# Optimization experiments

Measured on AMD Instinct MI355X. Metric: run time of the kernel, lower is better.

## Reference

```python
import jax, jax.numpy as jnp
import numpy as np

N_NODES = 100000
N_EDGES = 1600000
D_IN = 64
D_HID = 64


def setup_inputs() -> dict:
    key = jax.random.key(0)
    k1, k2, k3, k4, k5 = jax.random.split(key, 5)
    x = jax.random.normal(k1, (N_NODES, D_IN), dtype=jnp.float32)
    edge_index = jax.random.randint(k2, (2, N_EDGES), 0, N_NODES, dtype=jnp.int64)
    edge_weight = jax.random.uniform(k3, (N_EDGES,), dtype=jnp.float32)
    # GCNConv glorot-initialized linear weights (bias=False)
    s0 = (6.0 / (D_IN + D_HID)) ** 0.5
    W0 = jax.random.uniform(k4, (D_IN, D_HID), minval=-s0, maxval=s0, dtype=jnp.float32)
    s1 = (6.0 / (D_HID + D_HID)) ** 0.5
    W1 = jax.random.uniform(k5, (D_HID, D_HID), minval=-s1, maxval=s1, dtype=jnp.float32)
    return {"x": x, "edge_index": edge_index, "edge_weight": edge_weight, "W0": W0, "W1": W1}


def _gcn_layer(x, W, src, dst, edge_weight, deg_inv_sqrt, n_nodes):
    # h = X W  (bias=False)
    h = x @ W  # [N, D]
    # symmetric normalization including self-loops (weight 1)
    norm = deg_inv_sqrt[src] * edge_weight * deg_inv_sqrt[dst]  # [E]
    # gather src features, scale, scatter-sum at dst
    agg = jax.ops.segment_sum(norm[:, None] * h[src], dst, num_segments=n_nodes)
    # self-loop contribution: norm_ii = deg_inv_sqrt[i]^2 * 1
    agg = agg + (deg_inv_sqrt * deg_inv_sqrt)[:, None] * h
    return jax.nn.relu(agg)  # dropout is identity in eval mode


def reference(x, edge_index, edge_weight, W0, W1):
    src, dst = edge_index[0], edge_index[1]
    # degree with self-loops (self-loop weight = 1), aggregated at dst (source_to_target flow)
    deg = jax.ops.segment_sum(edge_weight, dst, num_segments=N_NODES) + 1.0
    deg_inv_sqrt = jax.lax.rsqrt(deg)
    x = _gcn_layer(x, W0, src, dst, edge_weight, deg_inv_sqrt, N_NODES)
    x = _gcn_layer(x, W1, src, dst, edge_weight, deg_inv_sqrt, N_NODES)
    return x
```

## Files before the change

kernel.cpp:

```cpp
#include <hip/hip_runtime.h>
#include <hip/hip_fp16.h>

#define D 64
#define BSH 9
#define BSZ (1 << BSH)
#define PB 4096
#define CAPR 10240
#define CAPU (2 * CAPR)
#define FASTU (BSZ * 32)
#define SCAP 9216

__global__ __launch_bounds__(256) void initcur(int* __restrict__ ccur, int nbuck) {
    int t = threadIdx.x;
    if (t < nbuck) ccur[t] = t * CAPR;
    if (t == 255) ccur[255] = 0;
}

__global__ __launch_bounds__(512) void bucket1(const int* __restrict__ src,
                                               const int* __restrict__ dst,
                                               const float* __restrict__ ew,
                                               int* __restrict__ ccur,
                                               int2* __restrict__ pairs2,
                                               int E, int nbuck) {
    __shared__ int hist[512];
    __shared__ int lbase[512];
    __shared__ int gbase[512];
    __shared__ int wsum[8];
    __shared__ int w0s[PB];
    __shared__ int w1s[PB];
    __shared__ unsigned char bids[PB];
    int t = threadIdx.x;
    hist[t] = 0;
    __syncthreads();
    int e0 = blockIdx.x * PB;
    int cnt = min(PB, E - e0);
    int b[8], lr[8], w0[8], w1[8];
    int i8 = t * 8;
    bool full8 = (i8 + 8 <= cnt);
    if (full8) {
        int4   sa = *(const int4*)&src[e0 + i8];
        int4   sb = *(const int4*)&src[e0 + i8 + 4];
        int4   da = *(const int4*)&dst[e0 + i8];
        int4   db = *(const int4*)&dst[e0 + i8 + 4];
        float4 wa = *(const float4*)&ew[e0 + i8];
        float4 wb = *(const float4*)&ew[e0 + i8 + 4];
        int ss[8] = {sa.x, sa.y, sa.z, sa.w, sb.x, sb.y, sb.z, sb.w};
        int ds[8] = {da.x, da.y, da.z, da.w, db.x, db.y, db.z, db.w};
        float wv[8] = {wa.x, wa.y, wa.z, wa.w, wb.x, wb.y, wb.z, wb.w};
#pragma unroll
        for (int k = 0; k < 8; ++k) {
            b[k]  = ds[k] >> BSH;
            w0[k] = ss[k] | ((ds[k] & (BSZ - 1)) << 17);
            w1[k] = __float_as_int(wv[k]);
            lr[k] = atomicAdd(&hist[b[k]], 1);
        }
    } else {
#pragma unroll
        for (int k = 0; k < 8; ++k) {
            int idx = i8 + k;
            if (idx < cnt) {
                int d = dst[e0 + idx];
                b[k]  = d >> BSH;
                w0[k] = src[e0 + idx] | ((d & (BSZ - 1)) << 17);
                w1[k] = __float_as_int(ew[e0 + idx]);
                lr[k] = atomicAdd(&hist[b[k]], 1);
            }
        }
    }
    __syncthreads();
    int hv = hist[t];
    int lane = t & 63, wv8 = t >> 6;
    int s = hv;
#pragma unroll
    for (int off = 1; off < 64; off <<= 1) {
        int u = __shfl_up(s, off, 64);
        if (lane >= off) s += u;
    }
    if (lane == 63) wsum[wv8] = s;
    __syncthreads();
    int woff = 0;
#pragma unroll
    for (int w = 0; w < 8; ++w) { int x = wsum[w]; if (w < wv8) woff += x; }
    int excl = s + woff - hv;
    lbase[t] = excl;
    if (t < nbuck && hv > 0) gbase[t] = atomicAdd(&ccur[t], hv);
    __syncthreads();
#pragma unroll
    for (int k = 0; k < 8; ++k) {
        int idx = i8 + k;
        if (idx < cnt) {
            int slot = lbase[b[k]] + lr[k];
            w0s[slot] = w0[k];
            w1s[slot] = w1[k];
            bids[slot] = (unsigned char)b[k];
        }
    }
    __syncthreads();
    for (int i = t; i < cnt; i += 512) {
        int bb = bids[i];
        int pos = gbase[bb] + (i - lbase[bb]);
        pairs2[pos] = make_int2(w0s[i], w1s[i]);
    }
}

__global__ __launch_bounds__(512) void sort2(int2* __restrict__ pairs2,
                                             unsigned int* __restrict__ fastU,
                                             const int* __restrict__ ccur,
                                             int2* __restrict__ extRng,
                                             unsigned int* __restrict__ extU,
                                             int* __restrict__ gext,
                                             float* __restrict__ dis,
                                             int N, int nbuck) {
    __shared__ int2 se[SCAP];
    __shared__ int cnt[512];
    __shared__ float sdeg[512];
    __shared__ int ebase[512];
    int b = blockIdx.x;
    int t = threadIdx.x;
    int baseR = b * CAPR;
    int baseU = b * CAPU;
    int cntb = min(ccur[b] - baseR, SCAP);
    for (int i = t; i < cntb; i += 512) se[i] = pairs2[baseR + i];
    cnt[t] = 0;
    sdeg[t] = 0.0f;
    __syncthreads();
    for (int i = t; i < cntb; i += 512) {
        int2 p = se[i];
        int dl = (p.x >> 17) & (BSZ - 1);
        int lr = atomicAdd(&cnt[dl], 1);
        atomicAdd(&sdeg[dl], __int_as_float(p.y));
        se[i].x = p.x | (lr << 26);
    }
    __syncthreads();
    int node = (b << BSH) + t;
    int cntv = cnt[t];
    int tot  = cntv + 1;
    int pc   = (tot <= 16) ? 16 : ((tot + 31) & ~31);
    int extLen = (pc > 32) ? (pc - 32) : 0;
    int extBase = 0;
    if (node < N && extLen > 0) extBase = atomicAdd(gext, extLen);
    float dloc = rsqrtf(sdeg[t] + 1.0f);
    __syncthreads();
    sdeg[t]  = dloc;
    ebase[t] = extBase;
    if (node < N) {
        int flag = (pc == 16) ? (1 << 30) : 0;
        extRng[node] = make_int2(extBase | flag, extBase + extLen);
        dis[node]    = dloc;
    }
    for (int i = t; i < FASTU; i += 512) fastU[baseU + i] = 0u;
    __syncthreads();
    for (int i = t; i < cntb; i += 512) {
        int2 p = se[i];
        int dl = (p.x >> 17) & (BSZ - 1);
        int s  = p.x & 0x1FFFF;
        int rank = ((unsigned int)p.x) >> 26;
        float w = __int_as_float(p.y) * sdeg[dl];
        unsigned int h = (unsigned int)__half_as_ushort(__float2half_rn(w));
        unsigned int packed = ((unsigned int)s << 15) | ((h + 1u) >> 1);
        if (rank < 32) fastU[baseU + dl * 32 + rank] = packed;
        else           extU[ebase[dl] + rank - 32]   = packed;
    }
    if (node < N) {
        unsigned int h = (unsigned int)__half_as_ushort(__float2half_rn(dloc));
        unsigned int selfp = ((unsigned int)node << 15) | ((h + 1u) >> 1);
        if (cntv < 32) fastU[baseU + t * 32 + cntv] = selfp;
        else           extU[extBase + cntv - 32]    = selfp;
        for (int i = cntv + 1 - 32; i < extLen; ++i) extU[extBase + i] = 0u;
    }
}

template<int HIN>
__global__ __launch_bounds__(256) void gemm64h(const void* __restrict__ Xv,
                                               const float* __restrict__ W,
                                               const float* __restrict__ dis,
                                               __half* __restrict__ Hb, int n) {
    __shared__ float Ws[64 * 64];
    __shared__ float Xs[16 * 64];
    for (int t = threadIdx.x; t < 64 * 64; t += 256) Ws[t] = W[t];
    int row0 = blockIdx.x * 16;
    for (int t = threadIdx.x; t < 16 * 64; t += 256) {
        int r = row0 + (t >> 6);
        float v = 0.0f;
        if (r < n) {
            if constexpr (HIN) v = __half2float(((const __half*)Xv)[r * 64 + (t & 63)]);
            else               v = ((const float*)Xv)[r * 64 + (t & 63)];
        }
        Xs[t] = v;
    }
    __syncthreads();
    int r  = threadIdx.x >> 4;
    int jc = (threadIdx.x & 15) * 4;
    float4 acc = make_float4(0.f, 0.f, 0.f, 0.f);
#pragma unroll
    for (int k = 0; k < 64; ++k) {
        float xv = Xs[r * 64 + k];
        float4 w = *(const float4*)&Ws[k * 64 + jc];
        acc.x += xv * w.x; acc.y += xv * w.y; acc.z += xv * w.z; acc.w += xv * w.w;
    }
    int rr = row0 + r;
    if (rr < n) {
        float ds = dis[rr];
        ushort4 pk;
        pk.x = __half_as_ushort(__float2half(ds * acc.x));
        pk.y = __half_as_ushort(__float2half(ds * acc.y));
        pk.z = __half_as_ushort(__float2half(ds * acc.z));
        pk.w = __half_as_ushort(__float2half(ds * acc.w));
        *(ushort4*)&Hb[rr * 64 + jc] = pk;
    }
}

__device__ __forceinline__ void acc_group(unsigned int pv, int g, int fl,
                                          const __half* __restrict__ Hb,
                                          __half2 a0[4], __half2 a1[4],
                                          __half2 a2[4], __half2 a3[4]) {
    unsigned int q0 = __shfl(pv, g, 64);
    unsigned int q1 = __shfl(pv, g + 8, 64);
    unsigned int q2 = __shfl(pv, g + 16, 64);
    unsigned int q3 = __shfl(pv, g + 24, 64);
    uint4 r0 = *(const uint4*)(Hb + (size_t)(q0 >> 15) * 64 + fl);
    uint4 r1 = *(const uint4*)(Hb + (size_t)(q1 >> 15) * 64 + fl);
    uint4 r2 = *(const uint4*)(Hb + (size_t)(q2 >> 15) * 64 + fl);
    uint4 r3 = *(const uint4*)(Hb + (size_t)(q3 >> 15) * 64 + fl);
    __half2 w0 = __half2half2(__ushort_as_half((unsigned short)((q0 & 0x7FFFu) << 1)));
    __half2 w1 = __half2half2(__ushort_as_half((unsigned short)((q1 & 0x7FFFu) << 1)));
    __half2 w2 = __half2half2(__ushort_as_half((unsigned short)((q2 & 0x7FFFu) << 1)));
    __half2 w3 = __half2half2(__ushort_as_half((unsigned short)((q3 & 0x7FFFu) << 1)));
    const __half2* h0 = (const __half2*)&r0;
    const __half2* h1 = (const __half2*)&r1;
    const __half2* h2 = (const __half2*)&r2;
    const __half2* h3 = (const __half2*)&r3;
#pragma unroll
    for (int k = 0; k < 4; ++k) {
        a0[k] = __hfma2(w0, h0[k], a0[k]);
        a1[k] = __hfma2(w1, h1[k], a1[k]);
        a2[k] = __hfma2(w2, h2[k], a2[k]);
        a3[k] = __hfma2(w3, h3[k], a3[k]);
    }
}

template<int HOUT>
__global__ __launch_bounds__(256) void gather64(const unsigned int* __restrict__ fastU,
                                                const unsigned int* __restrict__ extU,
                                                const int2* __restrict__ extRng,
                                                const __half* __restrict__ Hb,
                                                void* __restrict__ OUTv, int N) {
    int node = blockIdx.x * 4 + (threadIdx.x >> 6);
    if (node >= N) return;
    int lane = threadIdx.x & 63;
    int g    = lane >> 3;
    int fl   = (lane & 7) * 8;
    int l31  = lane & 31;
    int fbase = (node >> BSH) * CAPU + (node & (BSZ - 1)) * 32;
    unsigned int pv = fastU[fbase + l31];
    int2 er = extRng[node];
    bool small = (er.x & (1 << 30)) != 0;
    int eb = er.x & 0x3FFFFFFF;
    __half2 z = __float2half2_rn(0.0f);
    __half2 a0[4] = {z, z, z, z};
    __half2 a1[4] = {z, z, z, z};
    __half2 a2[4] = {z, z, z, z};
    __half2 a3[4] = {z, z, z, z};
    {
        unsigned int q0 = __shfl(pv, g, 64);
        unsigned int q1 = __shfl(pv, g + 8, 64);
        unsigned int q2 = __shfl(pv, g + 16, 64);
        unsigned int q3 = __shfl(pv, g + 24, 64);
        uint4 r0 = *(const uint4*)(Hb + (size_t)(q0 >> 15) * 64 + fl);
        uint4 r1 = *(const uint4*)(Hb + (size_t)(q1 >> 15) * 64 + fl);
        uint4 r2, r3;
        if (!small) {
            r2 = *(const uint4*)(Hb + (size_t)(q2 >> 15) * 64 + fl);
            r3 = *(const uint4*)(Hb + (size_t)(q3 >> 15) * 64 + fl);
        }
        __half2 w0 = __half2half2(__ushort_as_half((unsigned short)((q0 & 0x7FFFu) << 1)));
        __half2 w1 = __half2half2(__ushort_as_half((unsigned short)((q1 & 0x7FFFu) << 1)));
        const __half2* h0 = (const __half2*)&r0;
        const __half2* h1 = (const __half2*)&r1;
#pragma unroll
        for (int k = 0; k < 4; ++k) {
            a0[k] = __hfma2(w0, h0[k], a0[k]);
            a1[k] = __hfma2(w1, h1[k], a1[k]);
        }
        if (!small) {
            __half2 w2 = __half2half2(__ushort_as_half((unsigned short)((q2 & 0x7FFFu) << 1)));
            __half2 w3 = __half2half2(__ushort_as_half((unsigned short)((q3 & 0x7FFFu) << 1)));
            const __half2* h2 = (const __half2*)&r2;
            const __half2* h3 = (const __half2*)&r3;
#pragma unroll
            for (int k = 0; k < 4; ++k) {
                a2[k] = __hfma2(w2, h2[k], a2[k]);
                a3[k] = __hfma2(w3, h3[k], a3[k]);
            }
        }
    }
    for (int e = eb; e < er.y; e += 32)
        acc_group(extU[e + l31], g, fl, Hb, a0, a1, a2, a3);
    __half2 a[4];
#pragma unroll
    for (int k = 0; k < 4; ++k)
        a[k] = __hadd2(__hadd2(a0[k], a1[k]), __hadd2(a2[k], a3[k]));
#pragma unroll
    for (int m = 8; m < 64; m <<= 1) {
#pragma unroll
        for (int k = 0; k < 4; ++k) {
            unsigned u = __shfl_xor(*(unsigned*)&a[k], m, 64);
            a[k] = __hadd2(a[k], *(__half2*)&u);
        }
    }
    if (g < 2) {
        int o = g * 2;
        float2 f0 = __half22float2(a[o]);
        float2 f1 = __half22float2(a[o + 1]);
        float rx = fmaxf(f0.x, 0.0f), ry = fmaxf(f0.y, 0.0f);
        float rz = fmaxf(f1.x, 0.0f), rw = fmaxf(f1.y, 0.0f);
        if constexpr (HOUT) {
            ushort4 pk;
            pk.x = __half_as_ushort(__float2half(rx));
            pk.y = __half_as_ushort(__float2half(ry));
            pk.z = __half_as_ushort(__float2half(rz));
            pk.w = __half_as_ushort(__float2half(rw));
            *(ushort4*)&((__half*)OUTv)[node * 64 + fl + g * 4] = pk;
        } else {
            float4 vv = make_float4(rx, ry, rz, rw);
            *(float4*)&((float*)OUTv)[node * 64 + fl + g * 4] = vv;
        }
    }
}

extern "C" void kernel_launch(void* const* d_in, const int* in_sizes, int n_in,
                              void* d_out, int out_size, void* d_ws, size_t ws_size,
                              hipStream_t stream) {
    const float* x  = (const float*)d_in[0];
    const int*   ei = (const int*)d_in[1];
    const float* ew = (const float*)d_in[2];
    const float* W0 = (const float*)d_in[3];
    const float* W1 = (const float*)d_in[4];
    float* out = (float*)d_out;

    const int N = in_sizes[0] / D;
    const int E = in_sizes[2];
    const int* src = ei;
    const int* dst = ei + E;

    const int nbuck = (N + BSZ - 1) >> BSH;
    const int Na = (N + 1 + 255) & ~255;

    float* dis     = (float*)d_ws;
    int2*  extRng  = (int2*)((int*)d_ws + Na);
    int*   ccur    = (int*)d_ws + 3 * Na;
    int2*  pairs2  = (int2*)((int*)d_ws + 3 * Na + 1024);
    unsigned int* fastU = (unsigned int*)pairs2;
    __half* Hb     = (__half*)((int*)d_ws + 3 * Na + 1024 + (size_t)nbuck * CAPU);
    unsigned int* extU = (unsigned int*)(Hb + (size_t)N * D);
    __half* x1h    = (__half*)(extU + 262144);

    const int nb1 = (E + PB - 1) / PB;

    initcur<<<1, 256, 0, stream>>>(ccur, nbuck);
    bucket1<<<nb1, 512, 0, stream>>>(src, dst, ew, ccur, pairs2, E, nbuck);
    sort2<<<nbuck, 512, 0, stream>>>(pairs2, fastU, ccur, extRng, extU,
                                     ccur + 255, dis, N, nbuck);

    const int gemm_grid   = (N + 15) / 16;
    const int gather_grid = (N + 3) / 4;

    gemm64h<0><<<gemm_grid, 256, 0, stream>>>(x, W0, dis, Hb, N);
    gather64<1><<<gather_grid, 256, 0, stream>>>(fastU, extU, extRng, Hb, x1h, N);

    gemm64h<1><<<gemm_grid, 256, 0, stream>>>(x1h, W1, dis, Hb, N);
    gather64<0><<<gather_grid, 256, 0, stream>>>(fastU, extU, extRng, Hb, out, N);
}
```

Before: 190.2 us.

## Drop LDS staging in sort2, split fastU from pairs, two nodes per gather wave

sort2 no longer stages bucket pairs in a large LDS array. It reads them from global memory twice and assigns ranks with a second shared atomic counter pass, which frees LDS for occupancy and removes the SCAP cap. fastU now gets its own workspace region instead of aliasing pairs2, and x1h reuses the pairs2 area. The gather kernel processes two nodes per wave with independent accumulators to increase memory-level parallelism, at the cost of more registers and half as many blocks.

```diff
diff --git a/kernel.cpp b/kernel.cpp
--- a/kernel.cpp
+++ b/kernel.cpp
@@ -6,9 +6,7 @@
 #define BSZ (1 << BSH)
 #define PB 4096
 #define CAPR 10240
-#define CAPU (2 * CAPR)
 #define FASTU (BSZ * 32)
-#define SCAP 9216
 
 __global__ __launch_bounds__(256) void initcur(int* __restrict__ ccur, int nbuck) {
     int t = threadIdx.x;
@@ -103,7 +101,7 @@
     }
 }
 
-__global__ __launch_bounds__(512) void sort2(int2* __restrict__ pairs2,
+__global__ __launch_bounds__(512) void sort2(const int2* __restrict__ pairs2,
                                              unsigned int* __restrict__ fastU,
                                              const int* __restrict__ ccur,
                                              int2* __restrict__ extRng,
@@ -111,25 +109,24 @@
                                              int* __restrict__ gext,
                                              float* __restrict__ dis,
                                              int N, int nbuck) {
-    __shared__ int2 se[SCAP];
     __shared__ int cnt[512];
     __shared__ float sdeg[512];
+    __shared__ int cur[512];
     __shared__ int ebase[512];
     int b = blockIdx.x;
     int t = threadIdx.x;
     int baseR = b * CAPR;
-    int baseU = b * CAPU;
-    int cntb = min(ccur[b] - baseR, SCAP);
-    for (int i = t; i < cntb; i += 512) se[i] = pairs2[baseR + i];
+    int baseF = b * FASTU;
+    int cntb = min(ccur[b] - baseR, CAPR);
     cnt[t] = 0;
     sdeg[t] = 0.0f;
+    cur[t] = 0;
     __syncthreads();
     for (int i = t; i < cntb; i += 512) {
-        int2 p = se[i];
+        int2 p = pairs2[baseR + i];
         int dl = (p.x >> 17) & (BSZ - 1);
-        int lr = atomicAdd(&cnt[dl], 1);
+        atomicAdd(&cnt[dl], 1);
         atomicAdd(&sdeg[dl], __int_as_float(p.y));
-        se[i].x = p.x | (lr << 26);
     }
     __syncthreads();
     int node = (b << BSH) + t;
@@ -148,23 +145,24 @@
         extRng[node] = make_int2(extBase | flag, extBase + extLen);
         dis[node]    = dloc;
     }
-    for (int i = t; i < FASTU; i += 512) fastU[baseU + i] = 0u;
+    for (int i = t; i < FASTU; i += 512) fastU[baseF + i] = 0u;
     __syncthreads();
     for (int i = t; i < cntb; i += 512) {
-        int2 p = se[i];
+        int2 p = pairs2[baseR + i];
         int dl = (p.x >> 17) & (BSZ - 1);
         int s  = p.x & 0x1FFFF;
-        int rank = ((unsigned int)p.x) >> 26;
+        int rank = atomicAdd(&cur[dl], 1);
         float w = __int_as_float(p.y) * sdeg[dl];
         unsigned int h = (unsigned int)__half_as_ushort(__float2half_rn(w));
         unsigned int packed = ((unsigned int)s << 15) | ((h + 1u) >> 1);
-        if (rank < 32) fastU[baseU + dl * 32 + rank] = packed;
+        if (rank < 32) fastU[baseF + dl * 32 + rank] = packed;
         else           extU[ebase[dl] + rank - 32]   = packed;
     }
+    __syncthreads();
     if (node < N) {
         unsigned int h = (unsigned int)__half_as_ushort(__float2half_rn(dloc));
         unsigned int selfp = ((unsigned int)node << 15) | ((h + 1u) >> 1);
-        if (cntv < 32) fastU[baseU + t * 32 + cntv] = selfp;
+        if (cntv < 32) fastU[baseF + t * 32 + cntv] = selfp;
         else           extU[extBase + cntv - 32]    = selfp;
         for (int i = cntv + 1 - 32; i < extLen; ++i) extU[extBase + i] = 0u;
     }
@@ -239,63 +237,48 @@
     }
 }
 
+__device__ __forceinline__ void acc_main(unsigned int pv, bool small, int g, int fl,
+                                         const __half* __restrict__ Hb,
+                                         __half2 a0[4], __half2 a1[4],
+                                         __half2 a2[4], __half2 a3[4]) {
+    unsigned int q0 = __shfl(pv, g, 64);
+    unsigned int q1 = __shfl(pv, g + 8, 64);
+    unsigned int q2 = __shfl(pv, g + 16, 64);
+    unsigned int q3 = __shfl(pv, g + 24, 64);
+    uint4 r0 = *(const uint4*)(Hb + (size_t)(q0 >> 15) * 64 + fl);
+    uint4 r1 = *(const uint4*)(Hb + (size_t)(q1 >> 15) * 64 + fl);
+    uint4 r2, r3;
+    if (!small) {
+        r2 = *(const uint4*)(Hb + (size_t)(q2 >> 15) * 64 + fl);
+        r3 = *(const uint4*)(Hb + (size_t)(q3 >> 15) * 64 + fl);
+    }
+    __half2 w0 = __half2half2(__ushort_as_half((unsigned short)((q0 & 0x7FFFu) << 1)));
+    __half2 w1 = __half2half2(__ushort_as_half((unsigned short)((q1 & 0x7FFFu) << 1)));
+    const __half2* h0 = (const __half2*)&r0;
+    const __half2* h1 = (const __half2*)&r1;
+#pragma unroll
+    for (int k = 0; k < 4; ++k) {
+        a0[k] = __hfma2(w0, h0[k], a0[k]);
+        a1[k] = __hfma2(w1, h1[k], a1[k]);
+    }
+    if (!small) {
+        __half2 w2 = __half2half2(__ushort_as_half((unsigned short)((q2 & 0x7FFFu) << 1)));
+        __half2 w3 = __half2half2(__ushort_as_half((unsigned short)((q3 & 0x7FFFu) << 1)));
+        const __half2* h2 = (const __half2*)&r2;
+        const __half2* h3 = (const __half2*)&r3;
+#pragma unroll
+        for (int k = 0; k < 4; ++k) {
+            a2[k] = __hfma2(w2, h2[k], a2[k]);
+            a3[k] = __hfma2(w3, h3[k], a3[k]);
+        }
+    }
+}
+
 template<int HOUT>
-__global__ __launch_bounds__(256) void gather64(const unsigned int* __restrict__ fastU,
-                                                const unsigned int* __restrict__ extU,
-                                                const int2* __restrict__ extRng,
-                                                const __half* __restrict__ Hb,
-                                                void* __restrict__ OUTv, int N) {
-    int node = blockIdx.x * 4 + (threadIdx.x >> 6);
-    if (node >= N) return;
-    int lane = threadIdx.x & 63;
-    int g    = lane >> 3;
-    int fl   = (lane & 7) * 8;
-    int l31  = lane & 31;
-    int fbase = (node >> BSH) * CAPU + (node & (BSZ - 1)) * 32;
-    unsigned int pv = fastU[fbase + l31];
-    int2 er = extRng[node];
-    bool small = (er.x & (1 << 30)) != 0;
-    int eb = er.x & 0x3FFFFFFF;
-    __half2 z = __float2half2_rn(0.0f);
-    __half2 a0[4] = {z, z, z, z};
-    __half2 a1[4] = {z, z, z, z};
-    __half2 a2[4] = {z, z, z, z};
-    __half2 a3[4] = {z, z, z, z};
-    {
-        unsigned int q0 = __shfl(pv, g, 64);
-        unsigned int q1 = __shfl(pv, g + 8, 64);
-        unsigned int q2 = __shfl(pv, g + 16, 64);
-        unsigned int q3 = __shfl(pv, g + 24, 64);
-        uint4 r0 = *(const uint4*)(Hb + (size_t)(q0 >> 15) * 64 + fl);
-        uint4 r1 = *(const uint4*)(Hb + (size_t)(q1 >> 15) * 64 + fl);
-        uint4 r2, r3;
-        if (!small) {
-            r2 = *(const uint4*)(Hb + (size_t)(q2 >> 15) * 64 + fl);
-            r3 = *(const uint4*)(Hb + (size_t)(q3 >> 15) * 64 + fl);
-        }
-        __half2 w0 = __half2half2(__ushort_as_half((unsigned short)((q0 & 0x7FFFu) << 1)));
-        __half2 w1 = __half2half2(__ushort_as_half((unsigned short)((q1 & 0x7FFFu) << 1)));
-        const __half2* h0 = (const __half2*)&r0;
-        const __half2* h1 = (const __half2*)&r1;
-#pragma unroll
-        for (int k = 0; k < 4; ++k) {
-            a0[k] = __hfma2(w0, h0[k], a0[k]);
-            a1[k] = __hfma2(w1, h1[k], a1[k]);
-        }
-        if (!small) {
-            __half2 w2 = __half2half2(__ushort_as_half((unsigned short)((q2 & 0x7FFFu) << 1)));
-            __half2 w3 = __half2half2(__ushort_as_half((unsigned short)((q3 & 0x7FFFu) << 1)));
-            const __half2* h2 = (const __half2*)&r2;
-            const __half2* h3 = (const __half2*)&r3;
-#pragma unroll
-            for (int k = 0; k < 4; ++k) {
-                a2[k] = __hfma2(w2, h2[k], a2[k]);
-                a3[k] = __hfma2(w3, h3[k], a3[k]);
-            }
-        }
-    }
-    for (int e = eb; e < er.y; e += 32)
-        acc_group(extU[e + l31], g, fl, Hb, a0, a1, a2, a3);
+__device__ __forceinline__ void finish_node(__half2 a0[4], __half2 a1[4],
+                                            __half2 a2[4], __half2 a3[4],
+                                            int g, int fl,
+                                            void* __restrict__ OUTv, int node) {
     __half2 a[4];
 #pragma unroll
     for (int k = 0; k < 4; ++k)
@@ -328,6 +311,46 @@
     }
 }
 
+template<int HOUT>
+__global__ __launch_bounds__(256) void gather64(const unsigned int* __restrict__ fastU,
+                                                const unsigned int* __restrict__ extU,
+                                                const int2* __restrict__ extRng,
+                                                const __half* __restrict__ Hb,
+                                                void* __restrict__ OUTv, int N) {
+    int wv = threadIdx.x >> 6;
+    int node0 = blockIdx.x * 8 + wv;
+    if (node0 >= N) return;
+    int node1 = node0 + 4;
+    bool h1 = (node1 < N);
+    int lane = threadIdx.x & 63;
+    int g    = lane >> 3;
+    int fl   = (lane & 7) * 8;
+    int l31  = lane & 31;
+    int f0 = (node0 >> BSH) * FASTU + (node0 & (BSZ - 1)) * 32;
+    unsigned int pv0 = fastU[f0 + l31];
+    int2 er0 = extRng[node0];
+    int f1 = (node1 >> BSH) * FASTU + (node1 & (BSZ - 1)) * 32;
+    unsigned int pv1 = h1 ? fastU[f1 + l31] : 0u;
+    int2 er1 = h1 ? extRng[node1] : make_int2(1 << 30, 0);
+    bool small0 = (er0.x & (1 << 30)) != 0;
+    bool small1 = (er1.x & (1 << 30)) != 0;
+    int eb0 = er0.x & 0x3FFFFFFF;
+    int eb1 = er1.x & 0x3FFFFFFF;
+    __half2 z = __float2half2_rn(0.0f);
+    __half2 A0[4] = {z, z, z, z}, A1[4] = {z, z, z, z};
+    __half2 A2[4] = {z, z, z, z}, A3[4] = {z, z, z, z};
+    __half2 B0[4] = {z, z, z, z}, B1[4] = {z, z, z, z};
+    __half2 B2[4] = {z, z, z, z}, B3[4] = {z, z, z, z};
+    acc_main(pv0, small0, g, fl, Hb, A0, A1, A2, A3);
+    for (int e = eb0; e < er0.y; e += 32)
+        acc_group(extU[e + l31], g, fl, Hb, A0, A1, A2, A3);
+    acc_main(pv1, small1, g, fl, Hb, B0, B1, B2, B3);
+    for (int e = eb1; e < er1.y; e += 32)
+        acc_group(extU[e + l31], g, fl, Hb, B0, B1, B2, B3);
+    finish_node<HOUT>(A0, A1, A2, A3, g, fl, OUTv, node0);
+    if (h1) finish_node<HOUT>(B0, B1, B2, B3, g, fl, OUTv, node1);
+}
+
 extern "C" void kernel_launch(void* const* d_in, const int* in_sizes, int n_in,
                               void* d_out, int out_size, void* d_ws, size_t ws_size,
                               hipStream_t stream) {
@@ -350,10 +373,10 @@
     int2*  extRng  = (int2*)((int*)d_ws + Na);
     int*   ccur    = (int*)d_ws + 3 * Na;
     int2*  pairs2  = (int2*)((int*)d_ws + 3 * Na + 1024);
-    unsigned int* fastU = (unsigned int*)pairs2;
-    __half* Hb     = (__half*)((int*)d_ws + 3 * Na + 1024 + (size_t)nbuck * CAPU);
+    unsigned int* fastU = (unsigned int*)(pairs2 + (size_t)nbuck * CAPR);
+    __half* Hb     = (__half*)(fastU + (size_t)nbuck * FASTU);
     unsigned int* extU = (unsigned int*)(Hb + (size_t)N * D);
-    __half* x1h    = (__half*)(extU + 262144);
+    __half* x1h    = (__half*)pairs2;
 
     const int nb1 = (E + PB - 1) / PB;
 
@@ -363,7 +386,7 @@
                                      ccur + 255, dis, N, nbuck);
 
     const int gemm_grid   = (N + 15) / 16;
-    const int gather_grid = (N + 3) / 4;
+    const int gather_grid = (N + 7) / 8;
 
     gemm64h<0><<<gemm_grid, 256, 0, stream>>>(x, W0, dis, Hb, N);
     gather64<1><<<gather_grid, 256, 0, stream>>>(fastU, extU, extRng, Hb, x1h, N);
```

Result: no change. 190.6 us (+0.2%).
